# Kernel optimization log

Hardware: AMD Instinct MI355X
Metric: run time of the kernel (lower is better)

Reference implementation:

```python
import jax, jax.numpy as jnp
import numpy as np

N, D, H, O = 2048, 128, 256, 1  # batch, input_dim, hidden_dim, output_dim
LN_EPS = 1e-5


def setup_inputs() -> dict:
    key = jax.random.key(0)
    ks = jax.random.split(key, 10)
    s = lambda fan_in: 1.0 / np.sqrt(fan_in)
    return {
        "array": jax.random.normal(ks[0], (N, D), dtype=jnp.float32),
        # per-feature Linear(1, H) stacked: weight [D, H], bias [D, H]
        "W_in": jax.random.uniform(ks[1], (D, H), jnp.float32, -1.0, 1.0),
        "b_in": jax.random.uniform(ks[2], (D, H), jnp.float32, -1.0, 1.0),
        # FactorAttentionLayer (width D): W: Linear(D, D), V: Linear(D, 1), LayerNorm(D)
        "Wf": jax.random.uniform(ks[3], (D, D), jnp.float32, -s(D), s(D)),
        "bf": jax.random.uniform(ks[4], (D,), jnp.float32, -s(D), s(D)),
        "Vf": jax.random.uniform(ks[5], (D,), jnp.float32, -s(D), s(D)),
        "bv": jnp.zeros((), jnp.float32),
        "ln_g": jnp.ones((D,), jnp.float32),
        "ln_b": jnp.zeros((D,), jnp.float32),
        # fc_hidden: Linear(D*H, H); fc_output: Linear(H, O)  (stored as [in, out])
        "Wh": jax.random.uniform(ks[6], (D * H, H), jnp.float32, -s(D * H), s(D * H)),
        "bh": jax.random.uniform(ks[7], (H,), jnp.float32, -s(D * H), s(D * H)),
        "Wo": jax.random.uniform(ks[8], (H, O), jnp.float32, -s(H), s(H)),
        "bo": jax.random.uniform(ks[9], (O,), jnp.float32, -s(H), s(H)),
    }


def reference(array, W_in, b_in, Wf, bf, Vf, bv, ln_g, ln_b, Wh, bh, Wo, bo):
    # Fused per-feature Linear(1,H)+ReLU: [n, D, H]
    p = jax.nn.relu(array[:, :, None] * W_in[None] + b_in[None])
    # permute(0, 2, 1) -> [n, H, D]
    x = jnp.transpose(p, (0, 2, 1))
    # FactorAttention: tanh-linear, softmax over axis 1 (the H axis), residual mul, LayerNorm over D
    u = jnp.tanh(jnp.einsum('nhd,de->nhe', x, Wf) + bf)          # [n, H, D]
    scores = jnp.einsum('nhd,d->nh', u, Vf) + bv                  # [n, H]
    attn = jax.nn.softmax(scores, axis=1)[:, :, None]             # [n, H, 1]
    y = x + x * attn                                              # [n, H, D]
    mu = jnp.mean(y, axis=-1, keepdims=True)
    var = jnp.mean((y - mu) ** 2, axis=-1, keepdims=True)
    y = (y - mu) * jax.lax.rsqrt(var + LN_EPS) * ln_g + ln_b
    # flatten [n, H*D] and MLP head (dropout = identity in eval)
    xx = y.reshape(y.shape[0], -1)
    h = jax.nn.relu(xx @ Wh + bh)
    return h @ Wo + bo
```

## Files before the change

kernel.cpp:

```cpp
#include <hip/hip_runtime.h>

#define NB 2048
#define DD 128
#define HH 256
#define KF 32768
#define LN_EPS 1e-5f
#define KSPLIT 16
#define KSL (KF / KSPLIT)

typedef __attribute__((ext_vector_type(8))) short short8;
typedef __attribute__((ext_vector_type(4))) float float4_t;
typedef __attribute__((ext_vector_type(4))) float f4;

__device__ __forceinline__ unsigned short f2bf(float f) {
    unsigned int u = __builtin_bit_cast(unsigned int, f);
    u += 0x7fffu + ((u >> 16) & 1u);
    return (unsigned short)(u >> 16);
}

__device__ __forceinline__ unsigned int pkbf(float lo, float hi) {
    unsigned int r;
    asm("v_cvt_pk_bf16_f32 %0, %1, %2" : "=v"(r) : "v"(lo), "v"(hi));
    return r;
}

__device__ __forceinline__ void gl2lds16(const void* g, void* l) {
    __builtin_amdgcn_global_load_lds(
        (const __attribute__((address_space(1))) unsigned int*)g,
        (__attribute__((address_space(3))) unsigned int*)l, 16, 0, 0);
}

__global__ void stats_k(const float* __restrict__ arr, const float* __restrict__ Win,
                        const float* __restrict__ bin, float2* __restrict__ stats,
                        float* __restrict__ WinT, float* __restrict__ binT,
                        float* __restrict__ bias2) {
    __shared__ float a_s[2][128];
    __shared__ float tile[32][33];
    int bid = blockIdx.x;
    int t = threadIdx.x;

    if (bid >= 1024) {
        if (bid == 1088) { bias2[t] = 0.f; return; }
        int tid = bid - 1024;
        int mat = tid >> 5;
        int dt = (tid >> 3) & 3;
        int ht = tid & 7;
        const float* src = mat ? bin : Win;
        float* dst = mat ? binT : WinT;
        int c = t & 31, r = t >> 5;
#pragma unroll
        for (int rr = r; rr < 32; rr += 8)
            tile[rr][c] = src[(dt * 32 + rr) * 256 + ht * 32 + c];
        __syncthreads();
#pragma unroll
        for (int rr = r; rr < 32; rr += 8)
            dst[(ht * 32 + rr) * 128 + dt * 32 + c] = tile[c][rr];
        return;
    }

    int n0 = bid * 2;
    if (t < 256) a_s[t >> 7][t & 127] = arr[n0 * 128 + t];
    __syncthreads();
    int h = t;
    float sum[2] = {0.f, 0.f}, ssq[2] = {0.f, 0.f};
    for (int d = 0; d < 128; ++d) {
        float w = Win[d * 256 + h];
        float bb = bin[d * 256 + h];
#pragma unroll
        for (int q = 0; q < 2; ++q) {
            float x = fmaxf(fmaf(a_s[q][d], w, bb), 0.f);
            sum[q] += x;
            ssq[q] = fmaf(x, x, ssq[q]);
        }
    }
#pragma unroll
    for (int q = 0; q < 2; ++q) {
        float mu = sum[q] * (1.f / 128.f);
        float var = fmaxf(ssq[q] * (1.f / 128.f) - mu * mu, 0.f);
        float rs = rsqrtf(var + LN_EPS);
        stats[(long)(n0 + q) * HH + h] = make_float2(rs, mu * rs);
    }
}

__global__ void prep_b(const float* __restrict__ Wh, const float* __restrict__ g,
                       const float* __restrict__ beta, unsigned short* __restrict__ WhbT,
                       float* __restrict__ bias2) {
    __shared__ unsigned short tile[64][65];
    __shared__ float red[4][64];
    int kb = blockIdx.x;
    int jb = blockIdx.y;
    int t = threadIdx.x;
    int c = t & 63, r4 = t >> 6;
    int k0 = kb * 64;
    float bsum = 0.f;
    for (int rr = r4; rr < 64; rr += 4) {
        int k = k0 + rr, d = k & 127;
        float v = Wh[(long)k * 256 + jb * 64 + c];
        tile[rr][c] = f2bf(g[d] * v);
        bsum = fmaf(beta[d], v, bsum);
    }
    __syncthreads();
    for (int rr = r4; rr < 64; rr += 4)
        WhbT[(long)(jb * 64 + rr) * KF + k0 + c] = tile[c][rr];
    red[r4][c] = bsum;
    __syncthreads();
    if (r4 == 0)
        atomicAdd(&bias2[jb * 64 + c], red[0][c] + red[1][c] + red[2][c] + red[3][c]);
}

__global__ __launch_bounds__(512, 4) void gemm_f(
        const float* __restrict__ arr, const float* __restrict__ WinT,
        const float* __restrict__ binT, const float2* __restrict__ stats,
        const unsigned short* __restrict__ Bt,
        float* __restrict__ Cp) {
    __shared__ unsigned short Bs[2][128 * 32];
    __shared__ float2 Ss[128 * 18];
    int bid = blockIdx.x;
    int ks = bid >> 5;
    int mt = (bid >> 1) & 15;
    int nt = bid & 1;
    int m0 = mt * 128, n0 = nt * 128;
    long k0 = (long)ks * KSL;
    int h0 = ks * 16;
    int t = threadIdx.x;
    int lane = t & 63, wave = t >> 6;
    int wm = (wave >> 1) * 32;
    int wn = (wave & 1) * 64;
    int fr = lane & 15;
    int kch = lane >> 4;
    int fk8 = kch * 8;

    float4_t acc[2][4] = {};

    const unsigned short* Bab = Bt + (long)n0 * KF + k0;
    int j_s = t >> 2, kc_s = t & 3;
    long boff = (long)j_s * KF + (long)(((kc_s ^ (j_s & 3))) << 3);

    {
        int sr = t >> 2, sc = (t & 3) * 4;
        const float2* sp = stats + (long)(m0 + sr) * HH + h0 + sc;
        f4 v0 = *(const f4*)sp;
        f4 v1 = *(const f4*)(sp + 2);
        *(f4*)&Ss[sr * 18 + sc] = v0;
        *(f4*)&Ss[sr * 18 + sc + 2] = v1;
        gl2lds16(Bab + boff, &Bs[0][t * 8]);
    }
    int row0 = m0 + wm + fr;
    f4 aa[2][2];
    __syncthreads();

    for (int it = 0; it < 64; ++it) {
        int q = it >> 4, hl = it & 15, cur = it & 1;
        if (it < 63) {
            int itn = it + 1;
            int kap = (itn & 15) * 128 + (itn >> 4) * 32;
            gl2lds16(Bab + kap + boff, &Bs[cur ^ 1][t * 8]);
        }
        if (hl == 0) {
#pragma unroll
            for (int mi = 0; mi < 2; ++mi) {
                const float* ap = arr + (long)(row0 + mi * 16) * DD + q * 32 + fk8;
                aa[mi][0] = *(const f4*)ap;
                aa[mi][1] = *(const f4*)(ap + 4);
            }
        }
        short8 bfv[4];
#pragma unroll
        for (int ni = 0; ni < 4; ++ni) {
            int j = wn + ni * 16 + fr;
            bfv[ni] = *(const short8*)&Bs[cur][j * 32 + ((kch ^ (j & 3)) << 3)];
        }
        int h = h0 + hl;
        const float* wp = WinT + h * DD + q * 32 + fk8;
        const float* bp = binT + h * DD + q * 32 + fk8;
        f4 w0 = *(const f4*)wp, w1 = *(const f4*)(wp + 4);
        f4 v0 = *(const f4*)bp, v1 = *(const f4*)(bp + 4);
        short8 af[2];
#pragma unroll
        for (int mi = 0; mi < 2; ++mi) {
            float2 sv = Ss[(wm + mi * 16 + fr) * 18 + hl];
            float rs = sv.x, nm = -sv.y;
            float z0 = fmaf(fmaxf(fmaf(aa[mi][0][0], w0[0], v0[0]), 0.f), rs, nm);
            float z1 = fmaf(fmaxf(fmaf(aa[mi][0][1], w0[1], v0[1]), 0.f), rs, nm);
            float z2 = fmaf(fmaxf(fmaf(aa[mi][0][2], w0[2], v0[2]), 0.f), rs, nm);
            float z3 = fmaf(fmaxf(fmaf(aa[mi][0][3], w0[3], v0[3]), 0.f), rs, nm);
            float z4 = fmaf(fmaxf(fmaf(aa[mi][1][0], w1[0], v1[0]), 0.f), rs, nm);
            float z5 = fmaf(fmaxf(fmaf(aa[mi][1][1], w1[1], v1[1]), 0.f), rs, nm);
            float z6 = fmaf(fmaxf(fmaf(aa[mi][1][2], w1[2], v1[2]), 0.f), rs, nm);
            float z7 = fmaf(fmaxf(fmaf(aa[mi][1][3], w1[3], v1[3]), 0.f), rs, nm);
            union { short8 s; unsigned int u[4]; } pk;
            pk.u[0] = pkbf(z0, z1);
            pk.u[1] = pkbf(z2, z3);
            pk.u[2] = pkbf(z4, z5);
            pk.u[3] = pkbf(z6, z7);
            af[mi] = pk.s;
        }
#pragma unroll
        for (int mi = 0; mi < 2; ++mi)
#pragma unroll
            for (int ni = 0; ni < 4; ++ni)
                acc[mi][ni] = __builtin_amdgcn_mfma_f32_16x16x32_bf16(
                    af[mi], bfv[ni], acc[mi][ni], 0, 0, 0);
        if (it < 63) __syncthreads();
    }

    int rb = (lane >> 4) * 4;
    float* Cb = Cp + (long)ks * NB * 256;
#pragma unroll
    for (int mi = 0; mi < 2; ++mi) {
#pragma unroll
        for (int ni = 0; ni < 4; ++ni) {
            int n = n0 + wn + ni * 16 + fr;
#pragma unroll
            for (int r = 0; r < 4; ++r) {
                int m = m0 + wm + mi * 16 + rb + r;
                Cb[(long)m * 256 + n] = acc[mi][ni][r];
            }
        }
    }
}

__global__ void finale(const float* __restrict__ Cp, const float* __restrict__ bh,
                       const float* __restrict__ Wo, const float* __restrict__ bo,
                       const float* __restrict__ bias2, float* __restrict__ out) {
    __shared__ float red[4];
    int n = blockIdx.x, t = threadIdx.x;
    int lane = t & 63, wave = t >> 6;
    float s = bh[t] + bias2[t];
    for (int sl = 0; sl < KSPLIT; ++sl)
        s += Cp[(long)sl * NB * 256 + (long)n * 256 + t];
    float v = fmaxf(s, 0.f) * Wo[t];
#pragma unroll
    for (int o = 32; o; o >>= 1) v += __shfl_down(v, o);
    if (lane == 0) red[wave] = v;
    __syncthreads();
    if (t == 0) out[n] = red[0] + red[1] + red[2] + red[3] + bo[0];
}

extern "C" void kernel_launch(void* const* d_in, const int* in_sizes, int n_in,
                              void* d_out, int out_size, void* d_ws, size_t ws_size,
                              hipStream_t stream) {
    const float* arr  = (const float*)d_in[0];
    const float* Win  = (const float*)d_in[1];
    const float* bin  = (const float*)d_in[2];
    const float* ln_g = (const float*)d_in[7];
    const float* ln_b = (const float*)d_in[8];
    const float* Wh   = (const float*)d_in[9];
    const float* bh   = (const float*)d_in[10];
    const float* Wo   = (const float*)d_in[11];
    const float* bo   = (const float*)d_in[12];
    float* out = (float*)d_out;

    char* ws = (char*)d_ws;
    unsigned short* WhbT = (unsigned short*)ws;
    float2* stats = (float2*)(ws + 16777216ull);
    float* Cp     = (float*)(ws + 20971520ull);
    float* WinT   = (float*)(ws + 54525952ull);
    float* binT   = (float*)(ws + 54657024ull);
    float* bias2  = (float*)(ws + 54788096ull);

    hipLaunchKernelGGL(stats_k, dim3(1089), dim3(256), 0, stream,
                       arr, Win, bin, stats, WinT, binT, bias2);
    hipLaunchKernelGGL(prep_b, dim3(512, 4), dim3(256), 0, stream,
                       Wh, ln_g, ln_b, WhbT, bias2);
    hipLaunchKernelGGL(gemm_f, dim3(512), dim3(512), 0, stream,
                       arr, WinT, binT, stats, WhbT, Cp);
    hipLaunchKernelGGL(finale, dim3(NB), dim3(256), 0, stream,
                       Cp, bh, Wo, bo, bias2, out);
}
```

Before: 205.2 us.

## Widen GEMM tile to full N, double K-split, reduce via atomics

Each GEMM block now covers all 256 output columns instead of 128, so the on-the-fly ReLU/LayerNorm A-fragment generation is done once per row tile rather than twice. The K-split doubles to 32, and blocks accumulate with float atomics into a single zeroed buffer instead of writing 16 partial slabs that the finale kernel re-reads. Per-block Win/bin slices are staged in LDS, and the B-tile XOR swizzle is dropped. The trade-off is heavy atomic traffic into L2, more LDS bank conflicts on B reads, and higher register and LDS use per block.

```diff
diff --git a/kernel.cpp b/kernel.cpp
--- a/kernel.cpp
+++ b/kernel.cpp
@@ -5,7 +5,7 @@
 #define HH 256
 #define KF 32768
 #define LN_EPS 1e-5f
-#define KSPLIT 16
+#define KSPLIT 32
 #define KSL (KF / KSPLIT)
 
 typedef __attribute__((ext_vector_type(8))) short short8;
@@ -33,7 +33,7 @@
 __global__ void stats_k(const float* __restrict__ arr, const float* __restrict__ Win,
                         const float* __restrict__ bin, float2* __restrict__ stats,
                         float* __restrict__ WinT, float* __restrict__ binT,
-                        float* __restrict__ bias2) {
+                        float* __restrict__ bias2, float* __restrict__ Cacc) {
     __shared__ float a_s[2][128];
     __shared__ float tile[32][33];
     int bid = blockIdx.x;
@@ -41,6 +41,12 @@
 
     if (bid >= 1024) {
         if (bid == 1088) { bias2[t] = 0.f; return; }
+        if (bid >= 1089) {
+            float* p = Cacc + (long)(bid - 1089) * 2048 + t * 8;
+            *(f4*)p = (f4){0.f, 0.f, 0.f, 0.f};
+            *(f4*)(p + 4) = (f4){0.f, 0.f, 0.f, 0.f};
+            return;
+        }
         int tid = bid - 1024;
         int mat = tid >> 5;
         int dt = (tid >> 3) & 3;
@@ -112,49 +118,57 @@
         const float* __restrict__ arr, const float* __restrict__ WinT,
         const float* __restrict__ binT, const float2* __restrict__ stats,
         const unsigned short* __restrict__ Bt,
-        float* __restrict__ Cp) {
-    __shared__ unsigned short Bs[2][128 * 32];
-    __shared__ float2 Ss[128 * 18];
+        float* __restrict__ Cacc) {
+    __shared__ unsigned short Bs[2][256 * 32];
+    __shared__ float Ws[8 * 128];
+    __shared__ float Vs[8 * 128];
+    __shared__ float2 Ss[128 * 9];
     int bid = blockIdx.x;
-    int ks = bid >> 5;
-    int mt = (bid >> 1) & 15;
-    int nt = bid & 1;
-    int m0 = mt * 128, n0 = nt * 128;
+    int mt = bid & 15;
+    int ks = bid >> 4;
+    int m0 = mt * 128;
     long k0 = (long)ks * KSL;
-    int h0 = ks * 16;
+    int h0 = ks * 8;
     int t = threadIdx.x;
     int lane = t & 63, wave = t >> 6;
     int wm = (wave >> 1) * 32;
-    int wn = (wave & 1) * 64;
+    int wn = (wave & 1) * 128;
     int fr = lane & 15;
     int kch = lane >> 4;
     int fk8 = kch * 8;
 
-    float4_t acc[2][4] = {};
-
-    const unsigned short* Bab = Bt + (long)n0 * KF + k0;
-    int j_s = t >> 2, kc_s = t & 3;
-    long boff = (long)j_s * KF + (long)(((kc_s ^ (j_s & 3))) << 3);
-
+    float4_t acc[2][8] = {};
+
+    const unsigned short* Bab = Bt + k0;
+    long boff0 = (long)(t >> 2) * KF + (long)(t & 3) * 8;
+    long boff1 = boff0 + 128l * KF;
+
+    if (t < 256) {
+        *(f4*)&Ws[t * 4] = *(const f4*)(WinT + h0 * 128 + t * 4);
+    } else {
+        *(f4*)&Vs[(t - 256) * 4] = *(const f4*)(binT + h0 * 128 + (t - 256) * 4);
+    }
     {
-        int sr = t >> 2, sc = (t & 3) * 4;
+        int sr = t >> 2, sc = (t & 3) * 2;
         const float2* sp = stats + (long)(m0 + sr) * HH + h0 + sc;
-        f4 v0 = *(const f4*)sp;
-        f4 v1 = *(const f4*)(sp + 2);
-        *(f4*)&Ss[sr * 18 + sc] = v0;
-        *(f4*)&Ss[sr * 18 + sc + 2] = v1;
-        gl2lds16(Bab + boff, &Bs[0][t * 8]);
-    }
+        float2 v0 = sp[0], v1 = sp[1];
+        Ss[sr * 9 + sc] = v0;
+        Ss[sr * 9 + sc + 1] = v1;
+    }
+    gl2lds16(Bab + boff0, &Bs[0][t * 8]);
+    gl2lds16(Bab + boff1, &Bs[0][(t + 512) * 8]);
+
     int row0 = m0 + wm + fr;
     f4 aa[2][2];
     __syncthreads();
 
-    for (int it = 0; it < 64; ++it) {
-        int q = it >> 4, hl = it & 15, cur = it & 1;
-        if (it < 63) {
+    for (int it = 0; it < 32; ++it) {
+        int q = it >> 3, hl = it & 7, cur = it & 1;
+        if (it < 31) {
             int itn = it + 1;
-            int kap = (itn & 15) * 128 + (itn >> 4) * 32;
-            gl2lds16(Bab + kap + boff, &Bs[cur ^ 1][t * 8]);
+            int kap = (itn & 7) * 128 + (itn >> 3) * 32;
+            gl2lds16(Bab + kap + boff0, &Bs[cur ^ 1][t * 8]);
+            gl2lds16(Bab + kap + boff1, &Bs[cur ^ 1][(t + 512) * 8]);
         }
         if (hl == 0) {
 #pragma unroll
@@ -164,21 +178,13 @@
                 aa[mi][1] = *(const f4*)(ap + 4);
             }
         }
-        short8 bfv[4];
-#pragma unroll
-        for (int ni = 0; ni < 4; ++ni) {
-            int j = wn + ni * 16 + fr;
-            bfv[ni] = *(const short8*)&Bs[cur][j * 32 + ((kch ^ (j & 3)) << 3)];
-        }
-        int h = h0 + hl;
-        const float* wp = WinT + h * DD + q * 32 + fk8;
-        const float* bp = binT + h * DD + q * 32 + fk8;
-        f4 w0 = *(const f4*)wp, w1 = *(const f4*)(wp + 4);
-        f4 v0 = *(const f4*)bp, v1 = *(const f4*)(bp + 4);
+        int wb = hl * 128 + q * 32 + fk8;
+        f4 w0 = *(const f4*)&Ws[wb], w1 = *(const f4*)&Ws[wb + 4];
+        f4 v0 = *(const f4*)&Vs[wb], v1 = *(const f4*)&Vs[wb + 4];
         short8 af[2];
 #pragma unroll
         for (int mi = 0; mi < 2; ++mi) {
-            float2 sv = Ss[(wm + mi * 16 + fr) * 18 + hl];
+            float2 sv = Ss[(wm + mi * 16 + fr) * 9 + hl];
             float rs = sv.x, nm = -sv.y;
             float z0 = fmaf(fmaxf(fmaf(aa[mi][0][0], w0[0], v0[0]), 0.f), rs, nm);
             float z1 = fmaf(fmaxf(fmaf(aa[mi][0][1], w0[1], v0[1]), 0.f), rs, nm);
@@ -196,39 +202,45 @@
             af[mi] = pk.s;
         }
 #pragma unroll
-        for (int mi = 0; mi < 2; ++mi)
-#pragma unroll
-            for (int ni = 0; ni < 4; ++ni)
-                acc[mi][ni] = __builtin_amdgcn_mfma_f32_16x16x32_bf16(
-                    af[mi], bfv[ni], acc[mi][ni], 0, 0, 0);
-        if (it < 63) __syncthreads();
+        for (int half = 0; half < 2; ++half) {
+            short8 bfv[4];
+#pragma unroll
+            for (int n4 = 0; n4 < 4; ++n4) {
+                int j = wn + (half * 4 + n4) * 16 + fr;
+                bfv[n4] = *(const short8*)&Bs[cur][j * 32 + fk8];
+            }
+#pragma unroll
+            for (int mi = 0; mi < 2; ++mi)
+#pragma unroll
+                for (int n4 = 0; n4 < 4; ++n4)
+                    acc[mi][half * 4 + n4] = __builtin_amdgcn_mfma_f32_16x16x32_bf16(
+                        af[mi], bfv[n4], acc[mi][half * 4 + n4], 0, 0, 0);
+        }
+        if (it < 31) __syncthreads();
     }
 
     int rb = (lane >> 4) * 4;
-    float* Cb = Cp + (long)ks * NB * 256;
 #pragma unroll
     for (int mi = 0; mi < 2; ++mi) {
 #pragma unroll
-        for (int ni = 0; ni < 4; ++ni) {
-            int n = n0 + wn + ni * 16 + fr;
+        for (int ni = 0; ni < 8; ++ni) {
+            int n = wn + ni * 16 + fr;
 #pragma unroll
             for (int r = 0; r < 4; ++r) {
                 int m = m0 + wm + mi * 16 + rb + r;
-                Cb[(long)m * 256 + n] = acc[mi][ni][r];
+                atomicAdd(&Cacc[(long)m * 256 + n], acc[mi][ni][r]);
             }
         }
     }
 }
 
-__global__ void finale(const float* __restrict__ Cp, const float* __restrict__ bh,
+__global__ void finale(const float* __restrict__ Cacc, const float* __restrict__ bh,
                        const float* __restrict__ Wo, const float* __restrict__ bo,
                        const float* __restrict__ bias2, float* __restrict__ out) {
     __shared__ float red[4];
     int n = blockIdx.x, t = threadIdx.x;
     int lane = t & 63, wave = t >> 6;
-    float s = bh[t] + bias2[t];
-    for (int sl = 0; sl < KSPLIT; ++sl)
-        s += Cp[(long)sl * NB * 256 + (long)n * 256 + t];
+    float s = bh[t] + bias2[t] + Cacc[(long)n * 256 + t];
     float v = fmaxf(s, 0.f) * Wo[t];
 #pragma unroll
     for (int o = 32; o; o >>= 1) v += __shfl_down(v, o);
@@ -254,17 +266,17 @@
     char* ws = (char*)d_ws;
     unsigned short* WhbT = (unsigned short*)ws;
     float2* stats = (float2*)(ws + 16777216ull);
-    float* Cp     = (float*)(ws + 20971520ull);
-    float* WinT   = (float*)(ws + 54525952ull);
-    float* binT   = (float*)(ws + 54657024ull);
-    float* bias2  = (float*)(ws + 54788096ull);
-
-    hipLaunchKernelGGL(stats_k, dim3(1089), dim3(256), 0, stream,
-                       arr, Win, bin, stats, WinT, binT, bias2);
+    float* Cacc   = (float*)(ws + 20971520ull);
+    float* WinT   = (float*)(ws + 23068672ull);
+    float* binT   = (float*)(ws + 23199744ull);
+    float* bias2  = (float*)(ws + 23330816ull);
+
+    hipLaunchKernelGGL(stats_k, dim3(1345), dim3(256), 0, stream,
+                       arr, Win, bin, stats, WinT, binT, bias2, Cacc);
     hipLaunchKernelGGL(prep_b, dim3(512, 4), dim3(256), 0, stream,
                        Wh, ln_g, ln_b, WhbT, bias2);
     hipLaunchKernelGGL(gemm_f, dim3(512), dim3(512), 0, stream,
-                       arr, WinT, binT, stats, WhbT, Cp);
+                       arr, WinT, binT, stats, WhbT, Cacc);
     hipLaunchKernelGGL(finale, dim3(NB), dim3(256), 0, stream,
-                       Cp, bh, Wo, bo, bias2, out);
-}
+                       Cacc, bh, Wo, bo, bias2, out);
+}
```

Measured after the change: 222.9 us. +8.6%, slower.
